# Kernel optimization log

Hardware: AMD Instinct MI355X
Metric: run time of the kernel (lower is better)

The kernel has to match this reference:

```python
import jax, jax.numpy as jnp
import numpy as np

NUM_LATENTS = 1
NUM_EMBEDDINGS = 2048
EMBEDDING_DIM = 64
DECAY = 0.99
EPS = 1e-5


def setup_inputs() -> dict:
    key = jax.random.key(0)
    k1, k2 = jax.random.split(key)
    x = jax.random.normal(k1, (65536, NUM_LATENTS * EMBEDDING_DIM), dtype=jnp.float32)
    embedding = jax.random.normal(k2, (NUM_LATENTS, NUM_EMBEDDINGS, EMBEDDING_DIM), dtype=jnp.float32)
    cluster_size = jnp.ones((NUM_LATENTS, NUM_EMBEDDINGS), dtype=jnp.float32)
    return {"input": x, "embedding": embedding, "cluster_size": cluster_size}


def reference(input, embedding, cluster_size):
    L, K, D = embedding.shape
    flat = input.reshape(-1, L, D)  # (N, L, D)
    # Squared euclidean distances (N, L, K), expanded form of (x - e)^2 sum over D
    x_sq = jnp.sum(flat * flat, axis=-1, keepdims=True)           # (N, L, 1)
    e_sq = jnp.sum(embedding * embedding, axis=-1)[None]          # (1, L, K)
    cross = jnp.einsum('nld,lkd->nlk', flat, embedding)           # (N, L, K)
    distances = x_sq - 2.0 * cross + e_sq
    encoding_indices = jnp.argmin(distances, axis=-1)             # (N, L)
    # decode: gather codebook vectors
    quantized = embedding[jnp.arange(L)[None, :], encoding_indices]  # (N, L, D)
    encodings = jax.nn.one_hot(encoding_indices, K, dtype=input.dtype)  # (N, L, K)
    # --- EMA update (training branch, non-simple, laplace smoothing) ---
    onehot_sum = jnp.sum(encodings, axis=0)                       # (L, K)
    dw = jnp.einsum('nlk,nld->lkd', encodings, flat)              # (L, K, D)
    new_cluster_size = DECAY * cluster_size + (1.0 - DECAY) * onehot_sum
    n = jnp.sum(new_cluster_size, axis=-1, keepdims=True)
    cs = (new_cluster_size + EPS) / (n + K * EPS) * n
    new_embedding = DECAY * embedding + (1.0 - DECAY) * (dw / cs[..., None])
    # --- losses / outputs ---
    q = quantized.reshape(input.shape)
    commitment_loss = jnp.mean((q - input) ** 2)
    quantized_st = input + jax.lax.stop_gradient(q - input)
    avg_probs = jnp.mean(encodings, axis=0)                       # (L, K)
    perplexity = jnp.exp(-jnp.sum(avg_probs * jnp.log(avg_probs + 1e-10) / L))
    return (quantized_st, encodings, commitment_loss, perplexity, new_embedding, new_cluster_size)
```

## Files before the change

### kernel.cpp

```cpp
#include <hip/hip_runtime.h>
#include <math.h>

#define NROWS 65536
#define KEMB  2048
#define DIM   64
#define DECAYF 0.99f
#define OMDF   0.01f
#define EPSF   1e-5f

#define WS_DW    0
#define WS_CNT   131072
#define WS_LOSS  133120
#define WS_ESQ   133632
#define WS_IDX   135680

#define OUT_Q    0
#define OUT_ENC  4194304
#define OUT_LOSS 138412032
#define OUT_PERP 138412033
#define OUT_NE   138412034
#define OUT_NCS  138543106

typedef float f32x4 __attribute__((ext_vector_type(4)));

__global__ __launch_bounds__(256) void k0_prep(const float* __restrict__ E,
                                               float* __restrict__ ws) {
    int g = blockIdx.x * 256 + threadIdx.x;
    if (g == 0) ws[WS_LOSS] = 0.f;
    ((float4*)(ws + WS_DW))[g] = make_float4(0.f, 0.f, 0.f, 0.f);
    if (g < KEMB) {
        ((unsigned int*)ws)[WS_CNT + g] = 0u;
        const float4* e4 = (const float4*)(E + (size_t)g * DIM);
        float s0 = 0.f, s1 = 0.f, s2 = 0.f, s3 = 0.f;
#pragma unroll
        for (int j = 0; j < 16; j++) {
            float4 v = e4[j];
            s0 = fmaf(v.x, v.x, s0); s1 = fmaf(v.y, v.y, s1);
            s2 = fmaf(v.z, v.z, s2); s3 = fmaf(v.w, v.w, s3);
        }
        ws[WS_ESQ + g] = (s0 + s1) + (s2 + s3);
    }
}

__global__ __launch_bounds__(256, 2) void k1_main(const float* __restrict__ x,
                                                  const float* __restrict__ E,
                                                  float* __restrict__ ws,
                                                  float* __restrict__ out) {
    __shared__ float sxT[64 * 128];
    __shared__ float seT[32 * 256];
    __shared__ float sxq[256];

    const int t = threadIdx.x;
    const int b = blockIdx.x;
    const int tx = t & 15;
    const int ty = t >> 4;

    {
        const int rl = t & 127;
        const int dhi2 = t >> 7;
        const float4* x4 = (const float4*)x;
        float s0 = 0.f, s1 = 0.f, s2 = 0.f, s3 = 0.f;
#pragma unroll
        for (int i = 0; i < 8; i++) {
            int dc = dhi2 + 2 * i;
            float4 v = x4[((size_t)b * 128 + rl) * 16 + dc];
            sxT[(4 * dc + 0) * 128 + rl] = v.x;
            sxT[(4 * dc + 1) * 128 + rl] = v.y;
            sxT[(4 * dc + 2) * 128 + rl] = v.z;
            sxT[(4 * dc + 3) * 128 + rl] = v.w;
            s0 = fmaf(v.x, v.x, s0); s1 = fmaf(v.y, v.y, s1);
            s2 = fmaf(v.z, v.z, s2); s3 = fmaf(v.w, v.w, s3);
        }
        sxq[dhi2 * 128 + rl] = (s0 + s1) + (s2 + s3);
    }

    const int sbase = (((t >> 2) & 3) << 6) + ((t >> 4) << 2) + (t & 3);
    const float4* e4 = (const float4*)E;

    float4 pv[8];
#pragma unroll
    for (int j = 0; j < 8; j++)
        pv[j] = e4[(size_t)t * 16 + j];

    __syncthreads();

    float xsq[8];
#pragma unroll
    for (int rr = 0; rr < 8; rr++)
        xsq[rr] = sxq[ty * 8 + rr] + sxq[128 + ty * 8 + rr];

    float best[8];
    int bidx[8];
#pragma unroll
    for (int rr = 0; rr < 8; rr++) { best[rr] = 3.4e38f; bidx[rr] = 0; }

    f32x4* __restrict__ encz = (f32x4*)(out + OUT_ENC);

    for (int pass = 0; pass < 8; pass++) {
        float acc[8][16];
#pragma unroll
        for (int rr = 0; rr < 8; rr++)
#pragma unroll
            for (int m = 0; m < 16; m++) acc[rr][m] = 0.f;

        for (int dh = 0; dh < 2; dh++) {
            if (pass + dh) __syncthreads();
#pragma unroll
            for (int j = 0; j < 8; j++) {
                seT[(4 * j + 0) * 256 + sbase] = pv[j].x;
                seT[(4 * j + 1) * 256 + sbase] = pv[j].y;
                seT[(4 * j + 2) * 256 + sbase] = pv[j].z;
                seT[(4 * j + 3) * 256 + sbase] = pv[j].w;
            }
            __syncthreads();

            {
                int h = pass * 2 + dh + 1;
                if (h < 16) {
#pragma unroll
                    for (int j = 0; j < 8; j++)
                        pv[j] = e4[((size_t)((h >> 1) * 256 + t)) * 16 + (h & 1) * 8 + j];
                }
            }

            if (dh == 0) {
                f32x4 z = (f32x4)(0.f);
#pragma unroll
                for (int j = 0; j < 32; j++)
                    __builtin_nontemporal_store(z,
                        encz + (size_t)b * 65536 + pass * 8192 + j * 256 + t);
            }

            const float* xbase = sxT + dh * 32 * 128 + ty * 8;
            for (int dd = 0; dd < 32; dd++) {
                const float* sb = seT + dd * 256;
                f32x4 a0 = *(const f32x4*)(xbase + dd * 128);
                f32x4 a1 = *(const f32x4*)(xbase + dd * 128 + 4);
                f32x4 b0 = *(const f32x4*)(sb + tx * 4);
                f32x4 b1 = *(const f32x4*)(sb + 64 + tx * 4);
                f32x4 b2 = *(const f32x4*)(sb + 128 + tx * 4);
                f32x4 b3 = *(const f32x4*)(sb + 192 + tx * 4);
#pragma unroll
                for (int rr = 0; rr < 4; rr++) {
#pragma unroll
                    for (int cc = 0; cc < 4; cc++) {
                        acc[rr][cc]          = fmaf(a0[rr], b0[cc], acc[rr][cc]);
                        acc[rr][4 + cc]      = fmaf(a0[rr], b1[cc], acc[rr][4 + cc]);
                        acc[rr][8 + cc]      = fmaf(a0[rr], b2[cc], acc[rr][8 + cc]);
                        acc[rr][12 + cc]     = fmaf(a0[rr], b3[cc], acc[rr][12 + cc]);
                        acc[4 + rr][cc]      = fmaf(a1[rr], b0[cc], acc[4 + rr][cc]);
                        acc[4 + rr][4 + cc]  = fmaf(a1[rr], b1[cc], acc[4 + rr][4 + cc]);
                        acc[4 + rr][8 + cc]  = fmaf(a1[rr], b2[cc], acc[4 + rr][8 + cc]);
                        acc[4 + rr][12 + cc] = fmaf(a1[rr], b3[cc], acc[4 + rr][12 + cc]);
                    }
                }
            }
        }

        const float4* esq4 = (const float4*)(ws + WS_ESQ + pass * 256 + tx * 16);
        float4 eqv0 = esq4[0], eqv1 = esq4[1], eqv2 = esq4[2], eqv3 = esq4[3];
        float eq[16] = {eqv0.x, eqv0.y, eqv0.z, eqv0.w, eqv1.x, eqv1.y, eqv1.z, eqv1.w,
                        eqv2.x, eqv2.y, eqv2.z, eqv2.w, eqv3.x, eqv3.y, eqv3.z, eqv3.w};
        const int kb = pass * 256 + tx * 16;
#pragma unroll
        for (int rr = 0; rr < 8; rr++)
#pragma unroll
            for (int m = 0; m < 16; m++) {
                float dist = fmaf(-2.f, acc[rr][m], xsq[rr]) + eq[m];
                if (dist < best[rr]) { best[rr] = dist; bidx[rr] = kb + m; }
            }
    }

    int* sIdx = (int*)sxq;
#pragma unroll
    for (int rr = 0; rr < 8; rr++) {
        float bd = best[rr]; int bi = bidx[rr];
#pragma unroll
        for (int m = 1; m < 16; m <<= 1) {
            float od = __shfl_xor(bd, m, 64);
            int   oi = __shfl_xor(bi, m, 64);
            if (od < bd || (od == bd && oi < bi)) { bd = od; bi = oi; }
        }
        if (tx == 0) sIdx[ty * 8 + rr] = bi;
    }
    __syncthreads();

    if (t < 128) {
        const int row = b * 128 + t;
        const int bi = sIdx[t];
        ((int*)ws)[WS_IDX + row] = bi;
        atomicAdd(((unsigned int*)ws) + WS_CNT + bi, 1u);
        out[OUT_ENC + (size_t)row * KEMB + bi] = 1.0f;
        const float4* ebb = (const float4*)(E + (size_t)bi * DIM);
        const float4* xr4 = (const float4*)(x + (size_t)row * DIM);
        float4* qo = (float4*)(out + OUT_Q + (size_t)row * DIM);
        float l0 = 0.f, l1 = 0.f, l2 = 0.f, l3 = 0.f;
#pragma unroll
        for (int j = 0; j < 16; j++) {
            float4 ev = ebb[j];
            float4 xv = xr4[j];
            qo[j] = ev;
            float d0 = ev.x - xv.x, d1 = ev.y - xv.y;
            float d2 = ev.z - xv.z, d3 = ev.w - xv.w;
            l0 = fmaf(d0, d0, l0); l1 = fmaf(d1, d1, l1);
            l2 = fmaf(d2, d2, l2); l3 = fmaf(d3, d3, l3);
        }
        float lsum = (l0 + l1) + (l2 + l3);
#pragma unroll
        for (int o = 32; o; o >>= 1) lsum += __shfl_down(lsum, o, 64);
        if ((t & 63) == 0) unsafeAtomicAdd(ws + WS_LOSS, lsum);
    }
}

__global__ __launch_bounds__(256) void k2_dwD(const float* __restrict__ x,
                                              const int* __restrict__ idxp,
                                              float* __restrict__ ws) {
    __shared__ float tab[8][KEMB];
    const int t = threadIdx.x;
    const int b = blockIdx.x;
    const int d0 = (b & 7) * 8;
    const int rbase = (b >> 3) * 2048;

#pragma unroll
    for (int j = 0; j < 64; j++) ((float*)tab)[t + j * 256] = 0.f;
    __syncthreads();

    const int rt = t >> 3;
    const int dsub = t & 7;
    for (int i = 0; i < 64; i++) {
        int row = rbase + i * 32 + rt;
        int code = idxp[row];
        float v = x[(size_t)row * DIM + d0 + dsub];
        atomicAdd(&tab[dsub][code], v);
    }
    __syncthreads();

#pragma unroll
    for (int dl = 0; dl < 8; dl++)
#pragma unroll
        for (int j2 = 0; j2 < 8; j2++) {
            int k = t + j2 * 256;
            unsafeAtomicAdd(ws + WS_DW + (size_t)(d0 + dl) * KEMB + k, tab[dl][k]);
        }
}

__global__ __launch_bounds__(256) void k3_se(const float* __restrict__ cs_in,
                                             const float* __restrict__ E,
                                             const float* __restrict__ ws,
                                             float* __restrict__ out) {
    __shared__ float sred[8];
    __shared__ float sscale[16];
    __shared__ float s_n;
    const int t = threadIdx.x;
    const int b = blockIdx.x;
    const unsigned int* cnt = ((const unsigned int*)ws) + WS_CNT;

    float ln = 0.f, lent = 0.f;
#pragma unroll
    for (int j = 0; j < 8; j++) {
        int k = t * 8 + j;
        float c = (float)cnt[k];
        float ncs = DECAYF * cs_in[k] + OMDF * c;
        ln += ncs;
        float p = c * (1.0f / 65536.0f);
        lent = fmaf(p, logf(p + 1e-10f), lent);
    }
#pragma unroll
    for (int o = 32; o; o >>= 1) {
        ln += __shfl_down(ln, o, 64);
        lent += __shfl_down(lent, o, 64);
    }
    if ((t & 63) == 0) { sred[t >> 6] = ln; sred[4 + (t >> 6)] = lent; }
    __syncthreads();
    if (t == 0) {
        float n = (sred[0] + sred[1]) + (sred[2] + sred[3]);
        float ent = (sred[4] + sred[5]) + (sred[6] + sred[7]);
        s_n = n;
        if (b == 0) {
            out[OUT_LOSS] = ws[WS_LOSS] * (1.0f / 4194304.0f);
            out[OUT_PERP] = expf(-ent);
        }
    }
    __syncthreads();
    const float n = s_n;

    if (t < 16) {
        int k = b * 16 + t;
        float c = (float)cnt[k];
        float ncs = DECAYF * cs_in[k] + OMDF * c;
        out[OUT_NCS + k] = ncs;
        float cs = (ncs + EPSF) / (n + (float)KEMB * EPSF) * n;
        sscale[t] = OMDF / cs;
    }
    __syncthreads();

    const int kk = b * 16 + (t & 15);
    const int d4 = t >> 4;
    const float sc = sscale[t & 15];
    float dv0 = ws[WS_DW + (size_t)(d4 * 4 + 0) * KEMB + kk];
    float dv1 = ws[WS_DW + (size_t)(d4 * 4 + 1) * KEMB + kk];
    float dv2 = ws[WS_DW + (size_t)(d4 * 4 + 2) * KEMB + kk];
    float dv3 = ws[WS_DW + (size_t)(d4 * 4 + 3) * KEMB + kk];
    float4 e = ((const float4*)E)[kk * 16 + d4];
    float2 r0, r1;
    r0.x = fmaf(dv0, sc, DECAYF * e.x);
    r0.y = fmaf(dv1, sc, DECAYF * e.y);
    r1.x = fmaf(dv2, sc, DECAYF * e.z);
    r1.y = fmaf(dv3, sc, DECAYF * e.w);
    float2* o2 = (float2*)(out + OUT_NE);
    o2[(kk * 64 + d4 * 4) / 2 + 0] = r0;
    o2[(kk * 64 + d4 * 4) / 2 + 1] = r1;
}

extern "C" void kernel_launch(void* const* d_in, const int* in_sizes, int n_in,
                              void* d_out, int out_size, void* d_ws, size_t ws_size,
                              hipStream_t stream) {
    const float* x = (const float*)d_in[0];
    const float* E = (const float*)d_in[1];
    const float* cs = (const float*)d_in[2];
    float* out = (float*)d_out;
    float* ws = (float*)d_ws;
    const int* idxp = ((const int*)ws) + WS_IDX;

    hipLaunchKernelGGL(k0_prep, dim3(128), dim3(256), 0, stream, E, ws);
    hipLaunchKernelGGL(k1_main, dim3(512), dim3(256), 0, stream, x, E, ws, out);
    hipLaunchKernelGGL(k2_dwD, dim3(256), dim3(256), 0, stream, x, idxp, ws);
    hipLaunchKernelGGL(k3_se, dim3(128), dim3(256), 0, stream, cs, E, ws, out);
}
```

Baseline: 291.9 us.

## Halve k1 block to 64 rows with 128 threads, restage codebook in quarter-D chunks

The distance/argmin kernel now uses 128-thread blocks covering 64 rows each, launched as 1024 blocks. Codebook staging in shared memory is split into four 16-dim chunks per pass instead of two 32-dim chunks, with each thread loading two codebook rows. This shrinks shared memory per block so more blocks can be resident, at the cost of more barriers and less reuse of each staged codebook tile. Separately, the dw scatter kernel now runs 64 blocks that each process 8192 rows, cutting the global atomic flushes fourfold but reducing parallelism.

Result: slower. 355.4 us (+21.8%).

```diff
diff --git a/kernel.cpp b/kernel.cpp
--- a/kernel.cpp
+++ b/kernel.cpp
@@ -42,13 +42,13 @@
     }
 }
 
-__global__ __launch_bounds__(256, 2) void k1_main(const float* __restrict__ x,
+__global__ __launch_bounds__(128, 2) void k1_main(const float* __restrict__ x,
                                                   const float* __restrict__ E,
                                                   float* __restrict__ ws,
                                                   float* __restrict__ out) {
-    __shared__ float sxT[64 * 128];
-    __shared__ float seT[32 * 256];
-    __shared__ float sxq[256];
+    __shared__ float sxT[64 * 64];
+    __shared__ float seT[16 * 256];
+    __shared__ float sxq[128];
 
     const int t = threadIdx.x;
     const int b = blockIdx.x;
@@ -56,38 +56,42 @@
     const int ty = t >> 4;
 
     {
-        const int rl = t & 127;
-        const int dhi2 = t >> 7;
+        const int rl = t & 63;
+        const int dhi2 = t >> 6;
         const float4* x4 = (const float4*)x;
         float s0 = 0.f, s1 = 0.f, s2 = 0.f, s3 = 0.f;
 #pragma unroll
         for (int i = 0; i < 8; i++) {
             int dc = dhi2 + 2 * i;
-            float4 v = x4[((size_t)b * 128 + rl) * 16 + dc];
-            sxT[(4 * dc + 0) * 128 + rl] = v.x;
-            sxT[(4 * dc + 1) * 128 + rl] = v.y;
-            sxT[(4 * dc + 2) * 128 + rl] = v.z;
-            sxT[(4 * dc + 3) * 128 + rl] = v.w;
+            float4 v = x4[((size_t)b * 64 + rl) * 16 + dc];
+            sxT[(4 * dc + 0) * 64 + rl] = v.x;
+            sxT[(4 * dc + 1) * 64 + rl] = v.y;
+            sxT[(4 * dc + 2) * 64 + rl] = v.z;
+            sxT[(4 * dc + 3) * 64 + rl] = v.w;
             s0 = fmaf(v.x, v.x, s0); s1 = fmaf(v.y, v.y, s1);
             s2 = fmaf(v.z, v.z, s2); s3 = fmaf(v.w, v.w, s3);
         }
-        sxq[dhi2 * 128 + rl] = (s0 + s1) + (s2 + s3);
-    }
-
-    const int sbase = (((t >> 2) & 3) << 6) + ((t >> 4) << 2) + (t & 3);
+        sxq[dhi2 * 64 + rl] = (s0 + s1) + (s2 + s3);
+    }
+
+    const int sbase0 = (((t >> 2) & 3) << 6) + ((t >> 4) << 2) + (t & 3);
+    const int c1 = t + 128;
+    const int sbase1 = (((c1 >> 2) & 3) << 6) + ((c1 >> 4) << 2) + (c1 & 3);
     const float4* e4 = (const float4*)E;
 
     float4 pv[8];
 #pragma unroll
-    for (int j = 0; j < 8; j++)
-        pv[j] = e4[(size_t)t * 16 + j];
+    for (int j = 0; j < 4; j++) {
+        pv[j]     = e4[(size_t)t * 16 + j];
+        pv[4 + j] = e4[(size_t)c1 * 16 + j];
+    }
 
     __syncthreads();
 
     float xsq[8];
 #pragma unroll
     for (int rr = 0; rr < 8; rr++)
-        xsq[rr] = sxq[ty * 8 + rr] + sxq[128 + ty * 8 + rr];
+        xsq[rr] = sxq[ty * 8 + rr] + sxq[64 + ty * 8 + rr];
 
     float best[8];
     int bidx[8];
@@ -103,39 +107,46 @@
 #pragma unroll
             for (int m = 0; m < 16; m++) acc[rr][m] = 0.f;
 
-        for (int dh = 0; dh < 2; dh++) {
-            if (pass + dh) __syncthreads();
-#pragma unroll
-            for (int j = 0; j < 8; j++) {
-                seT[(4 * j + 0) * 256 + sbase] = pv[j].x;
-                seT[(4 * j + 1) * 256 + sbase] = pv[j].y;
-                seT[(4 * j + 2) * 256 + sbase] = pv[j].z;
-                seT[(4 * j + 3) * 256 + sbase] = pv[j].w;
+        for (int q = 0; q < 4; q++) {
+            const int st = pass * 4 + q;
+            if (st) __syncthreads();
+#pragma unroll
+            for (int j = 0; j < 4; j++) {
+                seT[(4 * j + 0) * 256 + sbase0] = pv[j].x;
+                seT[(4 * j + 1) * 256 + sbase0] = pv[j].y;
+                seT[(4 * j + 2) * 256 + sbase0] = pv[j].z;
+                seT[(4 * j + 3) * 256 + sbase0] = pv[j].w;
+                seT[(4 * j + 0) * 256 + sbase1] = pv[4 + j].x;
+                seT[(4 * j + 1) * 256 + sbase1] = pv[4 + j].y;
+                seT[(4 * j + 2) * 256 + sbase1] = pv[4 + j].z;
+                seT[(4 * j + 3) * 256 + sbase1] = pv[4 + j].w;
             }
             __syncthreads();
 
             {
-                int h = pass * 2 + dh + 1;
-                if (h < 16) {
-#pragma unroll
-                    for (int j = 0; j < 8; j++)
-                        pv[j] = e4[((size_t)((h >> 1) * 256 + t)) * 16 + (h & 1) * 8 + j];
+                int h = st + 1;
+                if (h < 32) {
+#pragma unroll
+                    for (int j = 0; j < 4; j++) {
+                        pv[j]     = e4[((size_t)((h >> 2) * 256 + t)) * 16 + (h & 3) * 4 + j];
+                        pv[4 + j] = e4[((size_t)((h >> 2) * 256 + c1)) * 16 + (h & 3) * 4 + j];
+                    }
                 }
             }
 
-            if (dh == 0) {
+            {
                 f32x4 z = (f32x4)(0.f);
 #pragma unroll
-                for (int j = 0; j < 32; j++)
+                for (int j = 0; j < 8; j++)
                     __builtin_nontemporal_store(z,
-                        encz + (size_t)b * 65536 + pass * 8192 + j * 256 + t);
-            }
-
-            const float* xbase = sxT + dh * 32 * 128 + ty * 8;
-            for (int dd = 0; dd < 32; dd++) {
+                        encz + (size_t)b * 32768 + pass * 4096 + (q * 8 + j) * 128 + t);
+            }
+
+            const float* xbase = sxT + q * 16 * 64 + ty * 8;
+            for (int dd = 0; dd < 16; dd++) {
                 const float* sb = seT + dd * 256;
-                f32x4 a0 = *(const f32x4*)(xbase + dd * 128);
-                f32x4 a1 = *(const f32x4*)(xbase + dd * 128 + 4);
+                f32x4 a0 = *(const f32x4*)(xbase + dd * 64);
+                f32x4 a1 = *(const f32x4*)(xbase + dd * 64 + 4);
                 f32x4 b0 = *(const f32x4*)(sb + tx * 4);
                 f32x4 b1 = *(const f32x4*)(sb + 64 + tx * 4);
                 f32x4 b2 = *(const f32x4*)(sb + 128 + tx * 4);
@@ -185,8 +196,8 @@
     }
     __syncthreads();
 
-    if (t < 128) {
-        const int row = b * 128 + t;
+    if (t < 64) {
+        const int row = b * 64 + t;
         const int bi = sIdx[t];
         ((int*)ws)[WS_IDX + row] = bi;
         atomicAdd(((unsigned int*)ws) + WS_CNT + bi, 1u);
@@ -208,7 +219,7 @@
         float lsum = (l0 + l1) + (l2 + l3);
 #pragma unroll
         for (int o = 32; o; o >>= 1) lsum += __shfl_down(lsum, o, 64);
-        if ((t & 63) == 0) unsafeAtomicAdd(ws + WS_LOSS, lsum);
+        if (t == 0) unsafeAtomicAdd(ws + WS_LOSS, lsum);
     }
 }
 
@@ -219,7 +230,7 @@
     const int t = threadIdx.x;
     const int b = blockIdx.x;
     const int d0 = (b & 7) * 8;
-    const int rbase = (b >> 3) * 2048;
+    const int rbase = (b >> 3) * 8192;
 
 #pragma unroll
     for (int j = 0; j < 64; j++) ((float*)tab)[t + j * 256] = 0.f;
@@ -227,7 +238,8 @@
 
     const int rt = t >> 3;
     const int dsub = t & 7;
-    for (int i = 0; i < 64; i++) {
+#pragma unroll 8
+    for (int i = 0; i < 256; i++) {
         int row = rbase + i * 32 + rt;
         int code = idxp[row];
         float v = x[(size_t)row * DIM + d0 + dsub];
@@ -323,7 +335,7 @@
     const int* idxp = ((const int*)ws) + WS_IDX;
 
     hipLaunchKernelGGL(k0_prep, dim3(128), dim3(256), 0, stream, E, ws);
-    hipLaunchKernelGGL(k1_main, dim3(512), dim3(256), 0, stream, x, E, ws, out);
-    hipLaunchKernelGGL(k2_dwD, dim3(256), dim3(256), 0, stream, x, idxp, ws);
+    hipLaunchKernelGGL(k1_main, dim3(1024), dim3(128), 0, stream, x, E, ws, out);
+    hipLaunchKernelGGL(k2_dwD, dim3(64), dim3(256), 0, stream, x, idxp, ws);
     hipLaunchKernelGGL(k3_se, dim3(128), dim3(256), 0, stream, cs, E, ws, out);
 }
```
